# Kernel optimization log

Measured on AMD Instinct MI355X. Metric: run time of the kernel, lower is better.

## Reference

```python
import jax, jax.numpy as jnp
import numpy as np

N_NODES = 100000
N_EDGES = 1600000
N_FEAT = 128
N_HID = 128
N_CLS = 40
DROP_P = 0.5


def setup_inputs() -> dict:
    key = jax.random.key(0)
    k1, k2, k3, k4 = jax.random.split(key, 4)
    x = jax.random.normal(k1, (N_NODES, N_FEAT), dtype=jnp.float32)
    edge_index = jax.random.randint(k2, (2, N_EDGES), 0, N_NODES, dtype=jnp.int32)
    W1 = jax.random.normal(k3, (N_FEAT, N_HID), dtype=jnp.float32) / np.sqrt(N_FEAT)
    b1 = jnp.zeros((N_HID,), dtype=jnp.float32)
    W2 = jax.random.normal(k4, (N_HID, N_CLS), dtype=jnp.float32) / np.sqrt(N_HID)
    b2 = jnp.zeros((N_CLS,), dtype=jnp.float32)
    return {"x": x, "edge_index": edge_index, "W1": W1, "b1": b1, "W2": W2, "b2": b2}


def _gcn_norm(edge_index, num_nodes):
    # add self-loops, then symmetric normalization D^-1/2 (A+I) D^-1/2
    loops = jnp.arange(num_nodes, dtype=edge_index.dtype)
    src = jnp.concatenate([edge_index[0], loops])
    dst = jnp.concatenate([edge_index[1], loops])
    deg = jax.ops.segment_sum(jnp.ones_like(dst, dtype=jnp.float32), dst,
                              num_segments=num_nodes)
    deg_isqrt = jax.lax.rsqrt(deg)  # deg >= 1 thanks to self-loops
    norm = deg_isqrt[src] * deg_isqrt[dst]  # [E+N]
    return src, dst, norm


def _gcn_conv(x, src, dst, norm, W, b, num_nodes):
    h = x @ W                                   # [N, out]
    msg = h[src] * norm[:, None]                # gather + scale, [E+N, out]
    out = jax.ops.segment_sum(msg, dst, num_segments=num_nodes)  # scatter-add
    return out + b


def reference(x, edge_index, W1, b1, W2, b2):
    num_nodes = x.shape[0]
    src, dst, norm = _gcn_norm(edge_index, num_nodes)
    h = _gcn_conv(x, src, dst, norm, W1, b1, num_nodes)
    h = jax.nn.relu(h)
    # dropout(p=0.5, training=True) with a fixed key for determinism
    keep = jax.random.uniform(jax.random.key(42), h.shape) >= DROP_P
    h = jnp.where(keep, h / (1.0 - DROP_P), 0.0)
    out = _gcn_conv(h, src, dst, norm, W2, b2, num_nodes)
    return out
```

## Files before the change

kernel.cpp:

```cpp
#include <hip/hip_runtime.h>

#define N_NODES 100000
#define N_EDGES 1600000
#define NBUCK 196
#define G1B 1563
#define FB 391
#define FEDGE 4096
#define BCAP 9216

typedef __attribute__((ext_vector_type(8))) short short8v;
typedef __attribute__((ext_vector_type(4))) float f32x4;

__device__ __forceinline__ unsigned pack_bf16(float a, float b){
  unsigned ua = __float_as_uint(a), ub = __float_as_uint(b);
  ua = ua + 0x7fffu + ((ua >> 16) & 1u);
  ub = ub + 0x7fffu + ((ub >> 16) & 1u);
  return (ua >> 16) | (ub & 0xffff0000u);
}
__device__ __forceinline__ unsigned short bf16_of(float a){
  unsigned ua = __float_as_uint(a);
  ua = ua + 0x7fffu + ((ua >> 16) & 1u);
  return (unsigned short)(ua >> 16);
}
__device__ __forceinline__ float bf_lo(unsigned u){ return __uint_as_float(u << 16); }
__device__ __forceinline__ float bf_hi(unsigned u){ return __uint_as_float(u & 0xffff0000u); }

__device__ __forceinline__ unsigned tf_rotl(unsigned x, int r){ return (x<<r)|(x>>(32-r)); }

__device__ __forceinline__ unsigned dropout_keep(unsigned e){
  unsigned x0 = 0u, x1 = e;
  const unsigned k0 = 0u, k1v = 42u;
  const unsigned k2 = 0x1BD11BDAu ^ k0 ^ k1v;
#define TF_R(r) { x0 += x1; x1 = tf_rotl(x1,(r)); x1 ^= x0; }
  x0 += k0; x1 += k1v;
  TF_R(13) TF_R(15) TF_R(26) TF_R(6)
  x0 += k1v; x1 += k2 + 1u;
  TF_R(17) TF_R(29) TF_R(16) TF_R(24)
  x0 += k2; x1 += k0 + 2u;
  TF_R(13) TF_R(15) TF_R(26) TF_R(6)
  x0 += k0; x1 += k1v + 3u;
  TF_R(17) TF_R(29) TF_R(16) TF_R(24)
  x0 += k1v; x1 += k2 + 4u;
  TF_R(13) TF_R(15) TF_R(26) TF_R(6)
  x0 += k2; x1 += k0 + 5u;
#undef TF_R
  return (x0 ^ x1) >> 31;
}

__global__ void k_init(const float* __restrict__ W1, const float* __restrict__ W2,
                       unsigned short* __restrict__ W1T, unsigned short* __restrict__ W2T48,
                       int* __restrict__ bcur2){
  int b = blockIdx.x, t = threadIdx.x;
  if (b < 64){
    int idx = b*256 + t;
    int k = idx >> 7, n = idx & 127;
    W1T[n*128 + k] = bf16_of(W1[idx]);
  } else {
    if (t < NBUCK) bcur2[t] = 0;
    for (int i = t; i < 48*128; i += 256){
      int c = i >> 7, k = i & 127;
      W2T48[c*128 + k] = (c < 40) ? bf16_of(W2[k*40 + c]) : (unsigned short)0;
    }
  }
}

__launch_bounds__(256)
__global__ void k_B(const float* __restrict__ x, const unsigned short* __restrict__ W1T,
                    unsigned short* __restrict__ h1u,
                    const int* __restrict__ src, const int* __restrict__ dst,
                    int* __restrict__ bcur2, unsigned* __restrict__ tmp, int N, int E){
  __shared__ int hist[NBUCK];
  int t = threadIdx.x;
  if (blockIdx.x < FB){
    int fb = blockIdx.x;
    for (int i = t; i < NBUCK; i += 256) hist[i] = 0;
    __syncthreads();
    int e0 = fb*FEDGE;
    #pragma unroll 4
    for (int j = 0; j < FEDGE/256; j++){
      int e = e0 + t + j*256;
      if (e < E) atomicAdd(&hist[dst[e] >> 9], 1);
    }
    __syncthreads();
    if (t < NBUCK){
      int c = hist[t];
      if (c > 0) hist[t] = t*BCAP + atomicAdd(&bcur2[t], c);
    }
    __syncthreads();
    #pragma unroll 4
    for (int j = 0; j < FEDGE/256; j++){
      int e = e0 + t + j*256;
      if (e < E){
        int d = dst[e], s = src[e];
        int p = atomicAdd(&hist[d >> 9], 1);
        tmp[p] = ((unsigned)(d & 511) << 17) | (unsigned)s;
      }
    }
    return;
  }
  int gb = blockIdx.x - FB;
  if (gb >= G1B) return;
  int w = t >> 6, l = t & 63;
  int lo = l & 15, hi = l >> 4;
  int rowA = gb*64 + w*16 + lo;
  int rA = (rowA < N) ? rowA : (N-1);
  const float4* xr = (const float4*)(x + (size_t)rA*128);

  short8v a[4];
  #pragma unroll
  for (int kk = 0; kk < 4; kk++){
    float4 f0 = xr[kk*8 + 2*hi];
    float4 f1 = xr[kk*8 + 2*hi + 1];
    union { short8v v; unsigned u[4]; } A;
    A.u[0] = pack_bf16(f0.x, f0.y);
    A.u[1] = pack_bf16(f0.z, f0.w);
    A.u[2] = pack_bf16(f1.x, f1.y);
    A.u[3] = pack_bf16(f1.z, f1.w);
    a[kk] = A.v;
  }
  int rowC0 = gb*64 + w*16 + hi*4;
  #pragma unroll
  for (int tt = 0; tt < 8; tt++){
    int n0 = tt*16;
    const uint4* brow = (const uint4*)(W1T + (n0 + lo)*128);
    f32x4 acc = {0.f, 0.f, 0.f, 0.f};
    #pragma unroll
    for (int kk = 0; kk < 4; kk++){
      union { short8v v; uint4 q; } B;
      B.q = brow[kk*4 + hi];
      acc = __builtin_amdgcn_mfma_f32_16x16x32_bf16(a[kk], B.v, acc, 0, 0, 0);
    }
    int colC = n0 + lo;
    #pragma unroll
    for (int r = 0; r < 4; r++){
      int rc = rowC0 + r;
      if (rc < N) h1u[(size_t)rc*128 + colC] = bf16_of(acc[r]);
    }
  }
}

__launch_bounds__(1024)
__global__ void k_hist(const unsigned* __restrict__ tmp, const int* __restrict__ bcur2,
                       int* __restrict__ degi, int* __restrict__ off,
                       float* __restrict__ dii, int N){
  __shared__ int cur[512];
  __shared__ int wtot[8];
  int b = blockIdx.x, t = threadIdx.x;
  if (t < 512) cur[t] = 0;
  __syncthreads();
  int m = bcur2[b];
  int base = b*BCAP;
  int node0 = b << 9;
  for (int i = t; i < m; i += 1024)
    atomicAdd(&cur[tmp[base + i] >> 17], 1);
  __syncthreads();
  if (t < 512){
    int v = cur[t];
    int lane = t & 63, w = t >> 6;
    int incl = v;
    for (int d = 1; d < 64; d <<= 1){
      int y = __shfl_up(incl, d);
      if (lane >= d) incl += y;
    }
    if (lane == 63) wtot[w] = incl;
    __syncthreads();
    int wb = 0;
    for (int i = 0; i < w; i++) wb += wtot[i];
    int excl = wb + incl - v;
    int n = node0 + t;
    if (n < N){
      degi[n] = v;
      off[n]  = base + excl;
      dii[n]  = rsqrtf((float)(v + 1));
    }
  }
}

__launch_bounds__(1024)
__global__ void k_csort(const unsigned* __restrict__ tmp, int2* __restrict__ csre,
                        const int* __restrict__ off, const int* __restrict__ bcur2,
                        const float* __restrict__ dii, int N){
  __shared__ int   cur[512];
  __shared__ float dl[512];
  int b = blockIdx.x, t = threadIdx.x;
  int node0 = b << 9;
  if (t < 512){
    int n = node0 + t;
    cur[t] = (n < N) ? off[n] : 0;
    dl[t]  = (n < N) ? dii[n] : 0.f;
  }
  __syncthreads();
  int m = bcur2[b];
  int base = b*BCAP;
  for (int i = t; i < m; i += 1024){
    unsigned e = tmp[base + i];
    int dloc = e >> 17;
    int s = e & 0x1FFFFu;
    float w = dii[s] * dl[dloc];
    int p = atomicAdd(&cur[dloc], 1);
    csre[p] = make_int2(s, __float_as_int(w));
  }
}

__launch_bounds__(256)
__global__ void k_agg1(const unsigned* __restrict__ h1g, unsigned* __restrict__ Bbg,
                       const int2* __restrict__ csre, const int* __restrict__ off,
                       const int* __restrict__ degi, const float* __restrict__ dii,
                       const float* __restrict__ b1, int N){
  int n = blockIdx.x*4 + (threadIdx.x >> 6);
  int lane = threadIdx.x & 63;
  if (n >= N) return;
  n = __builtin_amdgcn_readfirstlane(n);
  float din = dii[n];
  float s2 = din*din;
  unsigned su = h1g[(size_t)n*64 + lane];
  float a0 = bf_lo(su)*s2, a1 = bf_hi(su)*s2;
  int o = off[n], cnt = degi[n];
  int i = 0;
  for (; i + 8 <= cnt; i += 8){
    int2 e0 = csre[o+i+0], e1 = csre[o+i+1], e2 = csre[o+i+2], e3 = csre[o+i+3];
    int2 e4 = csre[o+i+4], e5 = csre[o+i+5], e6 = csre[o+i+6], e7 = csre[o+i+7];
    unsigned u0 = h1g[(size_t)e0.x*64 + lane];
    unsigned u1 = h1g[(size_t)e1.x*64 + lane];
    unsigned u2 = h1g[(size_t)e2.x*64 + lane];
    unsigned u3 = h1g[(size_t)e3.x*64 + lane];
    unsigned u4 = h1g[(size_t)e4.x*64 + lane];
    unsigned u5 = h1g[(size_t)e5.x*64 + lane];
    unsigned u6 = h1g[(size_t)e6.x*64 + lane];
    unsigned u7 = h1g[(size_t)e7.x*64 + lane];
    float w0 = __int_as_float(e0.y), w1 = __int_as_float(e1.y);
    float w2 = __int_as_float(e2.y), w3 = __int_as_float(e3.y);
    float w4 = __int_as_float(e4.y), w5 = __int_as_float(e5.y);
    float w6 = __int_as_float(e6.y), w7 = __int_as_float(e7.y);
    a0 = fmaf(bf_lo(u0), w0, a0); a1 = fmaf(bf_hi(u0), w0, a1);
    a0 = fmaf(bf_lo(u1), w1, a0); a1 = fmaf(bf_hi(u1), w1, a1);
    a0 = fmaf(bf_lo(u2), w2, a0); a1 = fmaf(bf_hi(u2), w2, a1);
    a0 = fmaf(bf_lo(u3), w3, a0); a1 = fmaf(bf_hi(u3), w3, a1);
    a0 = fmaf(bf_lo(u4), w4, a0); a1 = fmaf(bf_hi(u4), w4, a1);
    a0 = fmaf(bf_lo(u5), w5, a0); a1 = fmaf(bf_hi(u5), w5, a1);
    a0 = fmaf(bf_lo(u6), w6, a0); a1 = fmaf(bf_hi(u6), w6, a1);
    a0 = fmaf(bf_lo(u7), w7, a0); a1 = fmaf(bf_hi(u7), w7, a1);
  }
  for (; i < cnt; ++i){
    int2 e = csre[o+i];
    unsigned u = h1g[(size_t)e.x*64 + lane];
    float w = __int_as_float(e.y);
    a0 = fmaf(bf_lo(u), w, a0); a1 = fmaf(bf_hi(u), w, a1);
  }
  float2 bb = *(const float2*)(b1 + lane*2);
  a0 = fmaxf(a0 + bb.x, 0.f);
  a1 = fmaxf(a1 + bb.y, 0.f);
  unsigned e0i = (unsigned)n*128u + (unsigned)lane*2u;
  a0 = dropout_keep(e0i)      ? a0*2.f : 0.f;
  a1 = dropout_keep(e0i + 1u) ? a1*2.f : 0.f;
  Bbg[(size_t)n*64 + lane] = pack_bf16(a0, a1);
}

__launch_bounds__(256)
__global__ void k_gemm2(const unsigned* __restrict__ Bbg, const unsigned short* __restrict__ W2T48,
                        unsigned short* __restrict__ h2p, int N){
  int t = threadIdx.x;
  int w = t >> 6, l = t & 63;
  int lo = l & 15, hi = l >> 4;
  int rowA = blockIdx.x*64 + w*16 + lo;
  int rA = (rowA < N) ? rowA : (N-1);
  const uint4* ar = (const uint4*)(Bbg + (size_t)rA*64);

  short8v a[4];
  #pragma unroll
  for (int kk = 0; kk < 4; kk++){
    union { short8v v; uint4 q; } A;
    A.q = ar[kk*4 + hi];
    a[kk] = A.v;
  }
  int rowC0 = blockIdx.x*64 + w*16 + hi*4;
  #pragma unroll
  for (int tt = 0; tt < 3; tt++){
    int n0 = tt*16;
    const uint4* brow = (const uint4*)(W2T48 + (n0 + lo)*128);
    f32x4 acc = {0.f, 0.f, 0.f, 0.f};
    #pragma unroll
    for (int kk = 0; kk < 4; kk++){
      union { short8v v; uint4 q; } B;
      B.q = brow[kk*4 + hi];
      acc = __builtin_amdgcn_mfma_f32_16x16x32_bf16(a[kk], B.v, acc, 0, 0, 0);
    }
    int colC = n0 + lo;
    #pragma unroll
    for (int r = 0; r < 4; r++){
      int rc = rowC0 + r;
      if (rc < N) h2p[(size_t)rc*64 + colC] = bf16_of(acc[r]);
    }
  }
}

__launch_bounds__(256)
__global__ void k_agg2(const unsigned* __restrict__ h2p, float* __restrict__ out,
                       const int2* __restrict__ csre, const int* __restrict__ off,
                       const int* __restrict__ degi, const float* __restrict__ dii,
                       const float* __restrict__ b2, int N){
  int n = blockIdx.x*4 + (threadIdx.x >> 6);
  int lane31 = threadIdx.x & 31;
  int lane   = threadIdx.x & 63;
  if (n >= N) return;
  n = __builtin_amdgcn_readfirstlane(n);
  float din = dii[n];
  float sq = din*din;
  unsigned su = h2p[(size_t)n*32 + lane31];
  float a0 = bf_lo(su)*sq, a1 = bf_hi(su)*sq;
  int o = off[n], cnt = degi[n];
  int i = 0;
  for (; i + 8 <= cnt; i += 8){
    int2 e0 = csre[o+i+0], e1 = csre[o+i+1], e2 = csre[o+i+2], e3 = csre[o+i+3];
    int2 e4 = csre[o+i+4], e5 = csre[o+i+5], e6 = csre[o+i+6], e7 = csre[o+i+7];
    unsigned u0 = h2p[(size_t)e0.x*32 + lane31];
    unsigned u1 = h2p[(size_t)e1.x*32 + lane31];
    unsigned u2 = h2p[(size_t)e2.x*32 + lane31];
    unsigned u3 = h2p[(size_t)e3.x*32 + lane31];
    unsigned u4 = h2p[(size_t)e4.x*32 + lane31];
    unsigned u5 = h2p[(size_t)e5.x*32 + lane31];
    unsigned u6 = h2p[(size_t)e6.x*32 + lane31];
    unsigned u7 = h2p[(size_t)e7.x*32 + lane31];
    float w0 = __int_as_float(e0.y), w1 = __int_as_float(e1.y);
    float w2 = __int_as_float(e2.y), w3 = __int_as_float(e3.y);
    float w4 = __int_as_float(e4.y), w5 = __int_as_float(e5.y);
    float w6 = __int_as_float(e6.y), w7 = __int_as_float(e7.y);
    a0 = fmaf(bf_lo(u0), w0, a0); a1 = fmaf(bf_hi(u0), w0, a1);
    a0 = fmaf(bf_lo(u1), w1, a0); a1 = fmaf(bf_hi(u1), w1, a1);
    a0 = fmaf(bf_lo(u2), w2, a0); a1 = fmaf(bf_hi(u2), w2, a1);
    a0 = fmaf(bf_lo(u3), w3, a0); a1 = fmaf(bf_hi(u3), w3, a1);
    a0 = fmaf(bf_lo(u4), w4, a0); a1 = fmaf(bf_hi(u4), w4, a1);
    a0 = fmaf(bf_lo(u5), w5, a0); a1 = fmaf(bf_hi(u5), w5, a1);
    a0 = fmaf(bf_lo(u6), w6, a0); a1 = fmaf(bf_hi(u6), w6, a1);
    a0 = fmaf(bf_lo(u7), w7, a0); a1 = fmaf(bf_hi(u7), w7, a1);
  }
  for (; i < cnt; ++i){
    int2 e = csre[o+i];
    unsigned u = h2p[(size_t)e.x*32 + lane31];
    float w = __int_as_float(e.y);
    a0 = fmaf(bf_lo(u), w, a0); a1 = fmaf(bf_hi(u), w, a1);
  }
  if (lane < 20){
    float2 bb = *(const float2*)(b2 + lane*2);
    a0 += bb.x;
    a1 += bb.y;
    *(float2*)(out + (size_t)n*40 + lane*2) = make_float2(a0, a1);
  }
}

extern "C" void kernel_launch(void* const* d_in, const int* in_sizes, int n_in,
                              void* d_out, int out_size, void* d_ws, size_t ws_size,
                              hipStream_t stream){
  const float* x  = (const float*)d_in[0];
  const int*   ei = (const int*)  d_in[1];
  const float* W1 = (const float*)d_in[2];
  const float* b1 = (const float*)d_in[3];
  const float* W2 = (const float*)d_in[4];
  const float* b2 = (const float*)d_in[5];
  float* out = (float*)d_out;
  char* ws = (char*)d_ws;
  const int N = N_NODES, E = N_EDGES;
  const int* srcv = ei;
  const int* dstv = ei + E;

  int*   bcur2 = (int*)  (ws + 0);
  int*   off   = (int*)  (ws + 8192);
  int*   degi  = (int*)  (ws + 417792);
  float* dii   = (float*)(ws + 827392);
  unsigned short* W1T   = (unsigned short*)(ws + 1236992);
  unsigned short* W2T48 = (unsigned short*)(ws + 1269760);
  unsigned* tmp = (unsigned*)(ws + 1290240);
  int2*     csre= (int2*)   (ws + 8519680);
  unsigned short* h1u = (unsigned short*)(ws + 23068672);
  unsigned*       h1g = (unsigned*)      (ws + 23068672);
  unsigned short* h2p = (unsigned short*)(ws + 23068672);
  unsigned*       Bbg = (unsigned*)      (ws + 56623104);

  k_init<<<65, 256, 0, stream>>>(W1, W2, W1T, W2T48, bcur2);
  k_B<<<FB + G1B, 256, 0, stream>>>(x, W1T, h1u, srcv, dstv, bcur2, tmp, N, E);
  k_hist<<<NBUCK, 1024, 0, stream>>>(tmp, bcur2, degi, off, dii, N);
  k_csort<<<NBUCK, 1024, 0, stream>>>(tmp, csre, off, bcur2, dii, N);

  k_agg1 <<<N/4, 256, 0, stream>>>(h1g, Bbg, csre, off, degi, dii, b1, N);
  k_gemm2<<<(N + 63)/64, 256, 0, stream>>>(Bbg, W2T48, h2p, N);
  k_agg2 <<<N/4, 256, 0, stream>>>((const unsigned*)h2p, out, csre, off, degi, dii, b2, N);
}
```

Before: 210.5 us.

## Fuse layer-1 aggregation with layer-2 GEMM via shared-memory staging

Merges the first aggregation kernel and the second GEMM into one kernel. Each wave aggregates 16 nodes in sequence, writes the bf16 rows to LDS, then runs MFMA on them, so the intermediate activation is never written to or re-read from global memory and one launch is dropped. In exchange the grid shrinks from 25000 to 1563 blocks and each wave handles 16 nodes serially. That cuts parallelism for a latency-bound gather and may hurt latency hiding. h2p moves to a separate workspace region so it no longer aliases h1g.

```diff
diff --git a/kernel.cpp b/kernel.cpp
--- a/kernel.cpp
+++ b/kernel.cpp
@@ -203,74 +203,76 @@
 }
 
 __launch_bounds__(256)
-__global__ void k_agg1(const unsigned* __restrict__ h1g, unsigned* __restrict__ Bbg,
-                       const int2* __restrict__ csre, const int* __restrict__ off,
-                       const int* __restrict__ degi, const float* __restrict__ dii,
-                       const float* __restrict__ b1, int N){
-  int n = blockIdx.x*4 + (threadIdx.x >> 6);
-  int lane = threadIdx.x & 63;
-  if (n >= N) return;
-  n = __builtin_amdgcn_readfirstlane(n);
-  float din = dii[n];
-  float s2 = din*din;
-  unsigned su = h1g[(size_t)n*64 + lane];
-  float a0 = bf_lo(su)*s2, a1 = bf_hi(su)*s2;
-  int o = off[n], cnt = degi[n];
-  int i = 0;
-  for (; i + 8 <= cnt; i += 8){
-    int2 e0 = csre[o+i+0], e1 = csre[o+i+1], e2 = csre[o+i+2], e3 = csre[o+i+3];
-    int2 e4 = csre[o+i+4], e5 = csre[o+i+5], e6 = csre[o+i+6], e7 = csre[o+i+7];
-    unsigned u0 = h1g[(size_t)e0.x*64 + lane];
-    unsigned u1 = h1g[(size_t)e1.x*64 + lane];
-    unsigned u2 = h1g[(size_t)e2.x*64 + lane];
-    unsigned u3 = h1g[(size_t)e3.x*64 + lane];
-    unsigned u4 = h1g[(size_t)e4.x*64 + lane];
-    unsigned u5 = h1g[(size_t)e5.x*64 + lane];
-    unsigned u6 = h1g[(size_t)e6.x*64 + lane];
-    unsigned u7 = h1g[(size_t)e7.x*64 + lane];
-    float w0 = __int_as_float(e0.y), w1 = __int_as_float(e1.y);
-    float w2 = __int_as_float(e2.y), w3 = __int_as_float(e3.y);
-    float w4 = __int_as_float(e4.y), w5 = __int_as_float(e5.y);
-    float w6 = __int_as_float(e6.y), w7 = __int_as_float(e7.y);
-    a0 = fmaf(bf_lo(u0), w0, a0); a1 = fmaf(bf_hi(u0), w0, a1);
-    a0 = fmaf(bf_lo(u1), w1, a0); a1 = fmaf(bf_hi(u1), w1, a1);
-    a0 = fmaf(bf_lo(u2), w2, a0); a1 = fmaf(bf_hi(u2), w2, a1);
-    a0 = fmaf(bf_lo(u3), w3, a0); a1 = fmaf(bf_hi(u3), w3, a1);
-    a0 = fmaf(bf_lo(u4), w4, a0); a1 = fmaf(bf_hi(u4), w4, a1);
-    a0 = fmaf(bf_lo(u5), w5, a0); a1 = fmaf(bf_hi(u5), w5, a1);
-    a0 = fmaf(bf_lo(u6), w6, a0); a1 = fmaf(bf_hi(u6), w6, a1);
-    a0 = fmaf(bf_lo(u7), w7, a0); a1 = fmaf(bf_hi(u7), w7, a1);
-  }
-  for (; i < cnt; ++i){
-    int2 e = csre[o+i];
-    unsigned u = h1g[(size_t)e.x*64 + lane];
-    float w = __int_as_float(e.y);
-    a0 = fmaf(bf_lo(u), w, a0); a1 = fmaf(bf_hi(u), w, a1);
-  }
+__global__ void k_agg1g2(const unsigned* __restrict__ h1g,
+                         const unsigned short* __restrict__ W2T48,
+                         unsigned short* __restrict__ h2p,
+                         const int2* __restrict__ csre, const int* __restrict__ off,
+                         const int* __restrict__ degi, const float* __restrict__ dii,
+                         const float* __restrict__ b1, int N){
+  __shared__ unsigned Brow[64][68];
+  int t = threadIdx.x;
+  int w = t >> 6, lane = t & 63;
+  int nbase = blockIdx.x*64 + w*16;
   float2 bb = *(const float2*)(b1 + lane*2);
-  a0 = fmaxf(a0 + bb.x, 0.f);
-  a1 = fmaxf(a1 + bb.y, 0.f);
-  unsigned e0i = (unsigned)n*128u + (unsigned)lane*2u;
-  a0 = dropout_keep(e0i)      ? a0*2.f : 0.f;
-  a1 = dropout_keep(e0i + 1u) ? a1*2.f : 0.f;
-  Bbg[(size_t)n*64 + lane] = pack_bf16(a0, a1);
-}
-
-__launch_bounds__(256)
-__global__ void k_gemm2(const unsigned* __restrict__ Bbg, const unsigned short* __restrict__ W2T48,
-                        unsigned short* __restrict__ h2p, int N){
-  int t = threadIdx.x;
-  int w = t >> 6, l = t & 63;
-  int lo = l & 15, hi = l >> 4;
-  int rowA = blockIdx.x*64 + w*16 + lo;
-  int rA = (rowA < N) ? rowA : (N-1);
-  const uint4* ar = (const uint4*)(Bbg + (size_t)rA*64);
-
+
+  for (int j = 0; j < 16; j++){
+    int n = nbase + j;
+    unsigned pk = 0u;
+    if (n < N){
+      n = __builtin_amdgcn_readfirstlane(n);
+      float din = dii[n];
+      float s2 = din*din;
+      unsigned su = h1g[(size_t)n*64 + lane];
+      float a0 = bf_lo(su)*s2, a1 = bf_hi(su)*s2;
+      int o = off[n], cnt = degi[n];
+      int i = 0;
+      for (; i + 8 <= cnt; i += 8){
+        int2 e0 = csre[o+i+0], e1 = csre[o+i+1], e2 = csre[o+i+2], e3 = csre[o+i+3];
+        int2 e4 = csre[o+i+4], e5 = csre[o+i+5], e6 = csre[o+i+6], e7 = csre[o+i+7];
+        unsigned u0 = h1g[(size_t)e0.x*64 + lane];
+        unsigned u1 = h1g[(size_t)e1.x*64 + lane];
+        unsigned u2 = h1g[(size_t)e2.x*64 + lane];
+        unsigned u3 = h1g[(size_t)e3.x*64 + lane];
+        unsigned u4 = h1g[(size_t)e4.x*64 + lane];
+        unsigned u5 = h1g[(size_t)e5.x*64 + lane];
+        unsigned u6 = h1g[(size_t)e6.x*64 + lane];
+        unsigned u7 = h1g[(size_t)e7.x*64 + lane];
+        float w0 = __int_as_float(e0.y), w1 = __int_as_float(e1.y);
+        float w2 = __int_as_float(e2.y), w3 = __int_as_float(e3.y);
+        float w4 = __int_as_float(e4.y), w5 = __int_as_float(e5.y);
+        float w6 = __int_as_float(e6.y), w7 = __int_as_float(e7.y);
+        a0 = fmaf(bf_lo(u0), w0, a0); a1 = fmaf(bf_hi(u0), w0, a1);
+        a0 = fmaf(bf_lo(u1), w1, a0); a1 = fmaf(bf_hi(u1), w1, a1);
+        a0 = fmaf(bf_lo(u2), w2, a0); a1 = fmaf(bf_hi(u2), w2, a1);
+        a0 = fmaf(bf_lo(u3), w3, a0); a1 = fmaf(bf_hi(u3), w3, a1);
+        a0 = fmaf(bf_lo(u4), w4, a0); a1 = fmaf(bf_hi(u4), w4, a1);
+        a0 = fmaf(bf_lo(u5), w5, a0); a1 = fmaf(bf_hi(u5), w5, a1);
+        a0 = fmaf(bf_lo(u6), w6, a0); a1 = fmaf(bf_hi(u6), w6, a1);
+        a0 = fmaf(bf_lo(u7), w7, a0); a1 = fmaf(bf_hi(u7), w7, a1);
+      }
+      for (; i < cnt; ++i){
+        int2 e = csre[o+i];
+        unsigned u = h1g[(size_t)e.x*64 + lane];
+        float w0 = __int_as_float(e.y);
+        a0 = fmaf(bf_lo(u), w0, a0); a1 = fmaf(bf_hi(u), w0, a1);
+      }
+      a0 = fmaxf(a0 + bb.x, 0.f);
+      a1 = fmaxf(a1 + bb.y, 0.f);
+      unsigned e0i = (unsigned)n*128u + (unsigned)lane*2u;
+      a0 = dropout_keep(e0i)      ? a0*2.f : 0.f;
+      a1 = dropout_keep(e0i + 1u) ? a1*2.f : 0.f;
+      pk = pack_bf16(a0, a1);
+    }
+    Brow[w*16 + j][lane] = pk;
+  }
+  __syncthreads();
+
+  int lo = lane & 15, hi = lane >> 4;
   short8v a[4];
   #pragma unroll
   for (int kk = 0; kk < 4; kk++){
     union { short8v v; uint4 q; } A;
-    A.q = ar[kk*4 + hi];
+    A.q = *(const uint4*)(&Brow[w*16 + lo][16*kk + 4*hi]);
     a[kk] = A.v;
   }
   int rowC0 = blockIdx.x*64 + w*16 + hi*4;
@@ -373,15 +375,13 @@
   int2*     csre= (int2*)   (ws + 8519680);
   unsigned short* h1u = (unsigned short*)(ws + 23068672);
   unsigned*       h1g = (unsigned*)      (ws + 23068672);
-  unsigned short* h2p = (unsigned short*)(ws + 23068672);
-  unsigned*       Bbg = (unsigned*)      (ws + 56623104);
+  unsigned short* h2p = (unsigned short*)(ws + 56623104);
 
   k_init<<<65, 256, 0, stream>>>(W1, W2, W1T, W2T48, bcur2);
   k_B<<<FB + G1B, 256, 0, stream>>>(x, W1T, h1u, srcv, dstv, bcur2, tmp, N, E);
   k_hist<<<NBUCK, 1024, 0, stream>>>(tmp, bcur2, degi, off, dii, N);
   k_csort<<<NBUCK, 1024, 0, stream>>>(tmp, csre, off, bcur2, dii, N);
 
-  k_agg1 <<<N/4, 256, 0, stream>>>(h1g, Bbg, csre, off, degi, dii, b1, N);
-  k_gemm2<<<(N + 63)/64, 256, 0, stream>>>(Bbg, W2T48, h2p, N);
+  k_agg1g2<<<(N + 63)/64, 256, 0, stream>>>(h1g, W2T48, h2p, csre, off, degi, dii, b1, N);
   k_agg2 <<<N/4, 256, 0, stream>>>((const unsigned*)h2p, out, csre, off, degi, dii, b2, N);
 }
```

Result: no change. 211.2 us (+0.4%).
